# Optimization experiments

Hardware: AMD Instinct MI355X
Metric: run time of the kernel (lower is better)

Reference implementation:

```python
import jax, jax.numpy as jnp
import numpy as np

DELTA_V = 0.5
DELTA_D = 1.5
ALPHA = 1.0
BETA = 1.0
GAMMA = 0.001
K = 33  # label ids 0..32; 0 = background (ignored)
EPS = 1e-12


def setup_inputs() -> dict:
    key = jax.random.key(0)
    k1, k2 = jax.random.split(key)
    B, N, E = 8, 65536, 32
    embeddings = jax.random.normal(k1, (B, N, E), dtype=jnp.float32)
    labels = jax.random.randint(k2, (B, N), 0, K)
    return {"embeddings": embeddings, "labels": labels}


def reference(embeddings, labels):
    B, N, E = embeddings.shape
    dt = embeddings.dtype
    seg = (labels + jnp.arange(B)[:, None] * K).reshape(-1)  # (B*N,)

    # segment mean -> per-instance centers (B, K, E)
    sums = jax.ops.segment_sum(embeddings.reshape(B * N, E), seg, num_segments=B * K).reshape(B, K, E)
    counts = jax.ops.segment_sum(jnp.ones((B * N,), dtype=dt), seg, num_segments=B * K).reshape(B, K)
    centers = sums / jnp.maximum(counts, 1.0)[..., None]

    present = counts > 0
    present = present.at[:, 0].set(False)  # drop background label 0
    presf = present.astype(dt)
    n_inst = presf.sum(axis=1)  # (B,)

    # ---- variance term: per-point hinge distance to own center, segment-mean ----
    c_per_point = centers[jnp.arange(B)[:, None], labels]  # (B, N, E) gather
    d2 = ((embeddings - c_per_point) ** 2).sum(-1)
    dist = jnp.sqrt(jnp.maximum(d2, EPS))
    hinge = jnp.where(labels > 0, jnp.maximum(dist - DELTA_V, 0.0), 0.0)
    per_inst_sum = jax.ops.segment_sum(hinge.reshape(-1), seg, num_segments=B * K).reshape(B, K)
    per_inst_mean = per_inst_sum / jnp.maximum(counts, 1.0)
    variance_term = (per_inst_mean * presf).sum(1) / jnp.maximum(n_inst, 1.0)

    # ---- distance term: pairwise hinge between present instance centers ----
    diff2 = ((centers[:, :, None, :] - centers[:, None, :, :]) ** 2).sum(-1)  # (B,K,K)
    upper = jnp.triu(jnp.ones((K, K), dtype=bool), 1)[None]
    pair_valid = present[:, :, None] & present[:, None, :] & upper
    cd = jnp.sqrt(jnp.maximum(jnp.where(pair_valid, diff2, 1.0), EPS))
    pair_hinge = jnp.maximum(2.0 * DELTA_D - cd, 0.0) * pair_valid.astype(dt)
    n_pairs = n_inst * (n_inst - 1.0) * 0.5
    distance_term = pair_hinge.sum((1, 2)) / jnp.maximum(n_pairs, 1.0)

    # ---- regularization: mean L2 norm of present centers ----
    c_norm = jnp.sqrt(jnp.maximum((centers ** 2).sum(-1), EPS))
    reg_term = (c_norm * presf).sum(1) / jnp.maximum(n_inst, 1.0)

    per_batch = ALPHA * variance_term + BETA * distance_term + GAMMA * reg_term
    per_batch = jnp.where(n_inst > 0, per_batch, 0.0)
    return per_batch.sum() / B
```

## Files before the change

kernel.cpp:

```cpp
#include <hip/hip_runtime.h>
#include <math.h>

#define KC 33
#define ED 32
#define KE (KC * ED)
#define PAD 33

#define BPB_A 64
#define TPA 128
#define NSLOT 8
#define BPB_H 128
#define TPH 256


__global__ void k_zero(float* __restrict__ ws, int n, float* __restrict__ out) {
    int i = blockIdx.x * blockDim.x + threadIdx.x;
    if (i < n) ws[i] = 0.f;
    if (i == 0) out[0] = 0.f;
}

__global__ __launch_bounds__(256) void k_hist(const int* __restrict__ lab,
                                              float* __restrict__ counts, int N) {
    __shared__ float h[4 * KC];
    int t = threadIdx.x;
    int w = t >> 6;
    if (t < 4 * KC) h[t] = 0.f;
    __syncthreads();
    int b   = blockIdx.x >> 5;
    int blk = blockIdx.x & 31;
    const int4* l4 = (const int4*)(lab + (size_t)b * N + (size_t)blk * 2048);
    int4 a = l4[t];
    int4 c = l4[t + 256];
    float* hw = &h[w * KC];
    atomicAdd(&hw[a.x], 1.f); atomicAdd(&hw[a.y], 1.f);
    atomicAdd(&hw[a.z], 1.f); atomicAdd(&hw[a.w], 1.f);
    atomicAdd(&hw[c.x], 1.f); atomicAdd(&hw[c.y], 1.f);
    atomicAdd(&hw[c.z], 1.f); atomicAdd(&hw[c.w], 1.f);
    __syncthreads();
    if (t < KC)
        atomicAdd(&counts[b * KC + t], h[t] + h[KC + t] + h[2 * KC + t] + h[3 * KC + t]);
}

__global__ __launch_bounds__(256) void k_accum(const float* __restrict__ emb,
                                               const int* __restrict__ lab,
                                               float* __restrict__ sums, int N) {
    __shared__ float s_tile[TPA * PAD];
    __shared__ float s_priv[NSLOT * KE];
    __shared__ int   s_lab[TPA];
    int t = threadIdx.x;
    for (int i = t; i < NSLOT * KE; i += 256) s_priv[i] = 0.f;

    int b     = blockIdx.x / BPB_A;
    int blk   = blockIdx.x % BPB_A;
    int chunk = N / BPB_A;
    int e     = t & 31;
    int slot  = t >> 5;
    size_t pbase = (size_t)b * N + (size_t)blk * chunk;
    const int NT = chunk / TPA;

    const float4* g4 = (const float4*)(emb + pbase * ED);
    float4 r0 = g4[t], r1 = g4[t + 256], r2 = g4[t + 512], r3 = g4[t + 768];
    int rl = 0;
    if (t < TPA) rl = lab[pbase + t];
    __syncthreads();

    for (int tb = 0; tb < NT; tb++) {
        {
            int f, p, m;
            f = t;        p = f >> 3; m = (f & 7) * 4;
            { float* d = &s_tile[PAD * p + m]; d[0]=r0.x; d[1]=r0.y; d[2]=r0.z; d[3]=r0.w; }
            f = t + 256;  p = f >> 3; m = (f & 7) * 4;
            { float* d = &s_tile[PAD * p + m]; d[0]=r1.x; d[1]=r1.y; d[2]=r1.z; d[3]=r1.w; }
            f = t + 512;  p = f >> 3; m = (f & 7) * 4;
            { float* d = &s_tile[PAD * p + m]; d[0]=r2.x; d[1]=r2.y; d[2]=r2.z; d[3]=r2.w; }
            f = t + 768;  p = f >> 3; m = (f & 7) * 4;
            { float* d = &s_tile[PAD * p + m]; d[0]=r3.x; d[1]=r3.y; d[2]=r3.z; d[3]=r3.w; }
        }
        if (t < TPA) s_lab[t] = rl;
        __syncthreads();

        if (tb + 1 < NT) {
            const float4* gn = (const float4*)(emb + (pbase + (size_t)(tb + 1) * TPA) * ED);
            r0 = gn[t]; r1 = gn[t + 256]; r2 = gn[t + 512]; r3 = gn[t + 768];
            if (t < TPA) rl = lab[pbase + (size_t)(tb + 1) * TPA + t];
        }

        float* priv = &s_priv[slot * KE];
#pragma unroll
        for (int st = 0; st < TPA / NSLOT; st++) {
            int pt = st * NSLOT + slot;
            float x = s_tile[pt * PAD + e];
            int   k = s_lab[pt];
            priv[k * ED + e] += x;
        }
        __syncthreads();
    }

    for (int i = t; i < KE; i += 256) {
        float v = 0.f;
#pragma unroll
        for (int s = 0; s < NSLOT; s++) v += s_priv[s * KE + i];
        atomicAdd(&sums[(size_t)b * KE + i], v);
    }
}

__global__ __launch_bounds__(256) void k_hinge(const float* __restrict__ emb,
                                               const int* __restrict__ lab,
                                               const float* __restrict__ sums,
                                               const float* __restrict__ counts,
                                               float* __restrict__ var, int N) {
    __shared__ float s_tile[TPH * PAD];
    __shared__ float s_ctr[KC * PAD];
    __shared__ float s_cnt[KC];
    __shared__ float s_inv[KC];
    __shared__ int   s_lab[TPH];
    __shared__ float s_red[4];
    int t     = threadIdx.x;
    int b     = blockIdx.x / BPB_H;
    int blk   = blockIdx.x % BPB_H;
    int chunk = N / BPB_H;
    size_t pbase = (size_t)b * N + (size_t)blk * chunk;
    const int NT = chunk / TPH;

    const float4* g4 = (const float4*)(emb + pbase * ED);
    float4 r0 = g4[t],        r1 = g4[t + 256],  r2 = g4[t + 512],  r3 = g4[t + 768];
    float4 r4 = g4[t + 1024], r5 = g4[t + 1280], r6 = g4[t + 1536], r7 = g4[t + 1792];
    int rl = lab[pbase + t];

    if (t < KC) {
        float c = counts[b * KC + t];
        s_cnt[t] = fmaxf(c, 1.f);
        s_inv[t] = (t > 0 && c > 0.f) ? 1.f / fmaxf(c, 1.f) : 0.f;
    }
    __syncthreads();
    for (int i = t; i < KE; i += 256) {
        int k = i >> 5, e = i & 31;
        s_ctr[k * PAD + e] = sums[(size_t)b * KE + i] / s_cnt[k];
    }

    float hs = 0.f;
    for (int tb = 0; tb < NT; tb++) {
        {
            int f, p, m;
            f = t;         p = f >> 3; m = (f & 7) * 4;
            { float* d = &s_tile[PAD * p + m]; d[0]=r0.x; d[1]=r0.y; d[2]=r0.z; d[3]=r0.w; }
            f = t + 256;   p = f >> 3; m = (f & 7) * 4;
            { float* d = &s_tile[PAD * p + m]; d[0]=r1.x; d[1]=r1.y; d[2]=r1.z; d[3]=r1.w; }
            f = t + 512;   p = f >> 3; m = (f & 7) * 4;
            { float* d = &s_tile[PAD * p + m]; d[0]=r2.x; d[1]=r2.y; d[2]=r2.z; d[3]=r2.w; }
            f = t + 768;   p = f >> 3; m = (f & 7) * 4;
            { float* d = &s_tile[PAD * p + m]; d[0]=r3.x; d[1]=r3.y; d[2]=r3.z; d[3]=r3.w; }
            f = t + 1024;  p = f >> 3; m = (f & 7) * 4;
            { float* d = &s_tile[PAD * p + m]; d[0]=r4.x; d[1]=r4.y; d[2]=r4.z; d[3]=r4.w; }
            f = t + 1280;  p = f >> 3; m = (f & 7) * 4;
            { float* d = &s_tile[PAD * p + m]; d[0]=r5.x; d[1]=r5.y; d[2]=r5.z; d[3]=r5.w; }
            f = t + 1536;  p = f >> 3; m = (f & 7) * 4;
            { float* d = &s_tile[PAD * p + m]; d[0]=r6.x; d[1]=r6.y; d[2]=r6.z; d[3]=r6.w; }
            f = t + 1792;  p = f >> 3; m = (f & 7) * 4;
            { float* d = &s_tile[PAD * p + m]; d[0]=r7.x; d[1]=r7.y; d[2]=r7.z; d[3]=r7.w; }
        }
        s_lab[t] = rl;
        __syncthreads();

        if (tb + 1 < NT) {
            const float4* gn = (const float4*)(emb + (pbase + (size_t)(tb + 1) * TPH) * ED);
            r0 = gn[t];        r1 = gn[t + 256];  r2 = gn[t + 512];  r3 = gn[t + 768];
            r4 = gn[t + 1024]; r5 = gn[t + 1280]; r6 = gn[t + 1536]; r7 = gn[t + 1792];
            rl = lab[pbase + (size_t)(tb + 1) * TPH + t];
        }

        int   k  = s_lab[t];
        float iv = s_inv[k];
        const float* xr = &s_tile[t * PAD];
        const float* cr = &s_ctr[k * PAD];
        float d2 = 0.f;
#pragma unroll
        for (int j = 0; j < ED; j++) {
            float d = xr[j] - cr[j];
            d2 = fmaf(d, d, d2);
        }
        float dist = sqrtf(fmaxf(d2, 1e-12f));
        hs += fmaxf(dist - 0.5f, 0.f) * iv;
        __syncthreads();
    }

    hs += __shfl_xor(hs, 1);  hs += __shfl_xor(hs, 2);  hs += __shfl_xor(hs, 4);
    hs += __shfl_xor(hs, 8);  hs += __shfl_xor(hs, 16); hs += __shfl_xor(hs, 32);
    if ((t & 63) == 0) s_red[t >> 6] = hs;
    __syncthreads();
    if (t == 0)
        atomicAdd(&var[b], s_red[0] + s_red[1] + s_red[2] + s_red[3]);
}

__global__ __launch_bounds__(256) void k_final(const float* __restrict__ sums,
                                               const float* __restrict__ counts,
                                               const float* __restrict__ var,
                                               float* __restrict__ out, int B) {
    __shared__ float s_ctr[KE];
    __shared__ float s_cnt[KC];
    __shared__ float s_reg[KC];
    __shared__ int   s_prs[KC];
    __shared__ float s_red[256];
    int b = blockIdx.x;
    int t = threadIdx.x;

    if (t < KC) {
        float c = counts[b * KC + t];
        s_cnt[t] = fmaxf(c, 1.f);
        s_prs[t] = (t > 0 && c > 0.f) ? 1 : 0;
    }
    __syncthreads();
    for (int i = t; i < KE; i += 256)
        s_ctr[i] = sums[(size_t)b * KE + i] / s_cnt[i >> 5];
    __syncthreads();
    if (t < KC) {
        float n2 = 0.f;
        for (int e2 = 0; e2 < ED; e2++) { float c = s_ctr[t * ED + e2]; n2 += c * c; }
        s_reg[t] = s_prs[t] ? sqrtf(fmaxf(n2, 1e-12f)) : 0.f;
    }
    __syncthreads();

    float psum = 0.f;
    for (int q = t; q < KC * KC; q += 256) {
        int i = q / KC, j = q % KC;
        if (i < j && s_prs[i] && s_prs[j]) {
            float d2 = 0.f;
            for (int e2 = 0; e2 < ED; e2++) {
                float d = s_ctr[i * ED + e2] - s_ctr[j * ED + e2];
                d2 += d * d;
            }
            float cd = sqrtf(fmaxf(d2, 1e-12f));
            psum += fmaxf(3.0f - cd, 0.f);
        }
    }
    s_red[t] = psum;
    __syncthreads();
    for (int s = 128; s > 0; s >>= 1) {
        if (t < s) s_red[t] += s_red[t + s];
        __syncthreads();
    }

    if (t == 0) {
        float reg = 0.f; int n = 0;
        for (int k = 0; k < KC; k++) { reg += s_reg[k]; n += s_prs[k]; }
        float nf = (float)n;
        float variance_term = var[b] / fmaxf(nf, 1.f);
        float npairs = nf * (nf - 1.f) * 0.5f;
        float distance_term = s_red[0] / fmaxf(npairs, 1.f);
        float reg_term = reg / fmaxf(nf, 1.f);
        float pb = variance_term + distance_term + 0.001f * reg_term;
        if (n == 0) pb = 0.f;
        atomicAdd(out, pb / (float)B);
    }
}

extern "C" void kernel_launch(void* const* d_in, const int* in_sizes, int n_in,
                              void* d_out, int out_size, void* d_ws, size_t ws_size,
                              hipStream_t stream) {
    const float* emb = (const float*)d_in[0];
    const int*   lab = (const int*)d_in[1];
    float* out = (float*)d_out;

    const int B = 8;
    const int N = in_sizes[1] / B;

    float* sums   = (float*)d_ws;
    float* counts = sums + (size_t)B * KE;
    float* var    = counts + (size_t)B * KC;

    int zn = B * KE + B * KC + B;
    k_zero<<<(zn + 255) / 256, 256, 0, stream>>>(sums, zn, out);
    k_hist<<<B * 32, 256, 0, stream>>>(lab, counts, N);
    k_accum<<<B * BPB_A, 256, 0, stream>>>(emb, lab, sums, N);
    k_hinge<<<B * BPB_H, 256, 0, stream>>>(emb, lab, sums, counts, var, N);
    k_final<<<B, 256, 0, stream>>>(sums, counts, var, out, B);
}
```

Measured before the change: 133.4 us.

## Fuse histogram into accumulation, finalize via last-block, drop hinge LDS staging

The label histogram moves into the accumulation kernel, and the separate final kernel is replaced by a last-block-done counter inside the hinge kernel, which removes two launches. The hinge kernel now loads each point's 32 floats straight into registers (8 float4 per thread) and double-buffers them across iterations. This drops the shared-memory tile, its transposed stores and the per-iteration barriers. In exchange, per-thread strided loads are less coalesced, register pressure rises, and the fused finalize adds a threadfence and atomic counter.

```diff
diff --git a/kernel.cpp b/kernel.cpp
--- a/kernel.cpp
+++ b/kernel.cpp
@@ -19,36 +19,17 @@
     if (i == 0) out[0] = 0.f;
 }
 
-__global__ __launch_bounds__(256) void k_hist(const int* __restrict__ lab,
-                                              float* __restrict__ counts, int N) {
-    __shared__ float h[4 * KC];
-    int t = threadIdx.x;
-    int w = t >> 6;
-    if (t < 4 * KC) h[t] = 0.f;
-    __syncthreads();
-    int b   = blockIdx.x >> 5;
-    int blk = blockIdx.x & 31;
-    const int4* l4 = (const int4*)(lab + (size_t)b * N + (size_t)blk * 2048);
-    int4 a = l4[t];
-    int4 c = l4[t + 256];
-    float* hw = &h[w * KC];
-    atomicAdd(&hw[a.x], 1.f); atomicAdd(&hw[a.y], 1.f);
-    atomicAdd(&hw[a.z], 1.f); atomicAdd(&hw[a.w], 1.f);
-    atomicAdd(&hw[c.x], 1.f); atomicAdd(&hw[c.y], 1.f);
-    atomicAdd(&hw[c.z], 1.f); atomicAdd(&hw[c.w], 1.f);
-    __syncthreads();
-    if (t < KC)
-        atomicAdd(&counts[b * KC + t], h[t] + h[KC + t] + h[2 * KC + t] + h[3 * KC + t]);
-}
-
 __global__ __launch_bounds__(256) void k_accum(const float* __restrict__ emb,
                                                const int* __restrict__ lab,
-                                               float* __restrict__ sums, int N) {
+                                               float* __restrict__ sums,
+                                               float* __restrict__ counts, int N) {
     __shared__ float s_tile[TPA * PAD];
     __shared__ float s_priv[NSLOT * KE];
     __shared__ int   s_lab[TPA];
+    __shared__ float s_hist[2 * KC];
     int t = threadIdx.x;
     for (int i = t; i < NSLOT * KE; i += 256) s_priv[i] = 0.f;
+    if (t < 2 * KC) s_hist[t] = 0.f;
 
     int b     = blockIdx.x / BPB_A;
     int blk   = blockIdx.x % BPB_A;
@@ -76,7 +57,10 @@
             f = t + 768;  p = f >> 3; m = (f & 7) * 4;
             { float* d = &s_tile[PAD * p + m]; d[0]=r3.x; d[1]=r3.y; d[2]=r3.z; d[3]=r3.w; }
         }
-        if (t < TPA) s_lab[t] = rl;
+        if (t < TPA) {
+            s_lab[t] = rl;
+            atomicAdd(&s_hist[(t >> 6) * KC + rl], 1.f);
+        }
         __syncthreads();
 
         if (tb + 1 < NT) {
@@ -102,19 +86,32 @@
         for (int s = 0; s < NSLOT; s++) v += s_priv[s * KE + i];
         atomicAdd(&sums[(size_t)b * KE + i], v);
     }
-}
+    if (t < KC)
+        atomicAdd(&counts[b * KC + t], s_hist[t] + s_hist[KC + t]);
+}
+
+#define D2ACC(v, o) { float d_;                          \
+    d_ = (v).x - cr[(o)];     d2 = fmaf(d_, d_, d2);     \
+    d_ = (v).y - cr[(o) + 1]; d2 = fmaf(d_, d_, d2);     \
+    d_ = (v).z - cr[(o) + 2]; d2 = fmaf(d_, d_, d2);     \
+    d_ = (v).w - cr[(o) + 3]; d2 = fmaf(d_, d_, d2); }
 
 __global__ __launch_bounds__(256) void k_hinge(const float* __restrict__ emb,
                                                const int* __restrict__ lab,
                                                const float* __restrict__ sums,
                                                const float* __restrict__ counts,
-                                               float* __restrict__ var, int N) {
-    __shared__ float s_tile[TPH * PAD];
+                                               float* __restrict__ var,
+                                               unsigned* __restrict__ done,
+                                               float* __restrict__ out,
+                                               int N, int B) {
     __shared__ float s_ctr[KC * PAD];
     __shared__ float s_cnt[KC];
     __shared__ float s_inv[KC];
-    __shared__ int   s_lab[TPH];
+    __shared__ int   s_prs[KC];
+    __shared__ float s_reg[KC];
     __shared__ float s_red[4];
+    __shared__ float s_red2[256];
+    __shared__ int   s_last;
     int t     = threadIdx.x;
     int b     = blockIdx.x / BPB_H;
     int blk   = blockIdx.x % BPB_H;
@@ -122,100 +119,66 @@
     size_t pbase = (size_t)b * N + (size_t)blk * chunk;
     const int NT = chunk / TPH;
 
-    const float4* g4 = (const float4*)(emb + pbase * ED);
-    float4 r0 = g4[t],        r1 = g4[t + 256],  r2 = g4[t + 512],  r3 = g4[t + 768];
-    float4 r4 = g4[t + 1024], r5 = g4[t + 1280], r6 = g4[t + 1536], r7 = g4[t + 1792];
-    int rl = lab[pbase + t];
+    const float4* g0 = (const float4*)(emb + (pbase + t) * ED);
+    float4 x0 = g0[0], x1 = g0[1], x2 = g0[2], x3 = g0[3],
+           x4 = g0[4], x5 = g0[5], x6 = g0[6], x7 = g0[7];
+    int rk = lab[pbase + t];
 
     if (t < KC) {
         float c = counts[b * KC + t];
         s_cnt[t] = fmaxf(c, 1.f);
-        s_inv[t] = (t > 0 && c > 0.f) ? 1.f / fmaxf(c, 1.f) : 0.f;
+        int p = (t > 0 && c > 0.f) ? 1 : 0;
+        s_inv[t] = p ? 1.f / fmaxf(c, 1.f) : 0.f;
+        s_prs[t] = p;
     }
     __syncthreads();
     for (int i = t; i < KE; i += 256) {
         int k = i >> 5, e = i & 31;
         s_ctr[k * PAD + e] = sums[(size_t)b * KE + i] / s_cnt[k];
     }
+    __syncthreads();
 
     float hs = 0.f;
     for (int tb = 0; tb < NT; tb++) {
-        {
-            int f, p, m;
-            f = t;         p = f >> 3; m = (f & 7) * 4;
-            { float* d = &s_tile[PAD * p + m]; d[0]=r0.x; d[1]=r0.y; d[2]=r0.z; d[3]=r0.w; }
-            f = t + 256;   p = f >> 3; m = (f & 7) * 4;
-            { float* d = &s_tile[PAD * p + m]; d[0]=r1.x; d[1]=r1.y; d[2]=r1.z; d[3]=r1.w; }
-            f = t + 512;   p = f >> 3; m = (f & 7) * 4;
-            { float* d = &s_tile[PAD * p + m]; d[0]=r2.x; d[1]=r2.y; d[2]=r2.z; d[3]=r2.w; }
-            f = t + 768;   p = f >> 3; m = (f & 7) * 4;
-            { float* d = &s_tile[PAD * p + m]; d[0]=r3.x; d[1]=r3.y; d[2]=r3.z; d[3]=r3.w; }
-            f = t + 1024;  p = f >> 3; m = (f & 7) * 4;
-            { float* d = &s_tile[PAD * p + m]; d[0]=r4.x; d[1]=r4.y; d[2]=r4.z; d[3]=r4.w; }
-            f = t + 1280;  p = f >> 3; m = (f & 7) * 4;
-            { float* d = &s_tile[PAD * p + m]; d[0]=r5.x; d[1]=r5.y; d[2]=r5.z; d[3]=r5.w; }
-            f = t + 1536;  p = f >> 3; m = (f & 7) * 4;
-            { float* d = &s_tile[PAD * p + m]; d[0]=r6.x; d[1]=r6.y; d[2]=r6.z; d[3]=r6.w; }
-            f = t + 1792;  p = f >> 3; m = (f & 7) * 4;
-            { float* d = &s_tile[PAD * p + m]; d[0]=r7.x; d[1]=r7.y; d[2]=r7.z; d[3]=r7.w; }
-        }
-        s_lab[t] = rl;
-        __syncthreads();
-
+        float4 y0, y1, y2, y3, y4, y5, y6, y7;
+        int nk = 0;
         if (tb + 1 < NT) {
-            const float4* gn = (const float4*)(emb + (pbase + (size_t)(tb + 1) * TPH) * ED);
-            r0 = gn[t];        r1 = gn[t + 256];  r2 = gn[t + 512];  r3 = gn[t + 768];
-            r4 = gn[t + 1024]; r5 = gn[t + 1280]; r6 = gn[t + 1536]; r7 = gn[t + 1792];
-            rl = lab[pbase + (size_t)(tb + 1) * TPH + t];
-        }
-
-        int   k  = s_lab[t];
-        float iv = s_inv[k];
-        const float* xr = &s_tile[t * PAD];
-        const float* cr = &s_ctr[k * PAD];
+            const float4* gn = (const float4*)(emb + (pbase + (size_t)(tb + 1) * TPH + t) * ED);
+            y0 = gn[0]; y1 = gn[1]; y2 = gn[2]; y3 = gn[3];
+            y4 = gn[4]; y5 = gn[5]; y6 = gn[6]; y7 = gn[7];
+            nk = lab[pbase + (size_t)(tb + 1) * TPH + t];
+        }
+        const float* cr = &s_ctr[rk * PAD];
+        float iv = s_inv[rk];
         float d2 = 0.f;
-#pragma unroll
-        for (int j = 0; j < ED; j++) {
-            float d = xr[j] - cr[j];
-            d2 = fmaf(d, d, d2);
-        }
+        D2ACC(x0, 0)  D2ACC(x1, 4)  D2ACC(x2, 8)  D2ACC(x3, 12)
+        D2ACC(x4, 16) D2ACC(x5, 20) D2ACC(x6, 24) D2ACC(x7, 28)
         float dist = sqrtf(fmaxf(d2, 1e-12f));
         hs += fmaxf(dist - 0.5f, 0.f) * iv;
-        __syncthreads();
+        if (tb + 1 < NT) {
+            x0 = y0; x1 = y1; x2 = y2; x3 = y3;
+            x4 = y4; x5 = y5; x6 = y6; x7 = y7;
+            rk = nk;
+        }
     }
 
     hs += __shfl_xor(hs, 1);  hs += __shfl_xor(hs, 2);  hs += __shfl_xor(hs, 4);
     hs += __shfl_xor(hs, 8);  hs += __shfl_xor(hs, 16); hs += __shfl_xor(hs, 32);
     if ((t & 63) == 0) s_red[t >> 6] = hs;
     __syncthreads();
-    if (t == 0)
+    if (t == 0) {
         atomicAdd(&var[b], s_red[0] + s_red[1] + s_red[2] + s_red[3]);
-}
-
-__global__ __launch_bounds__(256) void k_final(const float* __restrict__ sums,
-                                               const float* __restrict__ counts,
-                                               const float* __restrict__ var,
-                                               float* __restrict__ out, int B) {
-    __shared__ float s_ctr[KE];
-    __shared__ float s_cnt[KC];
-    __shared__ float s_reg[KC];
-    __shared__ int   s_prs[KC];
-    __shared__ float s_red[256];
-    int b = blockIdx.x;
-    int t = threadIdx.x;
-
-    if (t < KC) {
-        float c = counts[b * KC + t];
-        s_cnt[t] = fmaxf(c, 1.f);
-        s_prs[t] = (t > 0 && c > 0.f) ? 1 : 0;
-    }
-    __syncthreads();
-    for (int i = t; i < KE; i += 256)
-        s_ctr[i] = sums[(size_t)b * KE + i] / s_cnt[i >> 5];
-    __syncthreads();
+        __threadfence();
+        unsigned old = atomicAdd(&done[b], 1u);
+        s_last = (old == (unsigned)(BPB_H - 1)) ? 1 : 0;
+    }
+    __syncthreads();
+    if (!s_last) return;
+
+    __threadfence();
     if (t < KC) {
         float n2 = 0.f;
-        for (int e2 = 0; e2 < ED; e2++) { float c = s_ctr[t * ED + e2]; n2 += c * c; }
+        for (int e2 = 0; e2 < ED; e2++) { float c = s_ctr[t * PAD + e2]; n2 += c * c; }
         s_reg[t] = s_prs[t] ? sqrtf(fmaxf(n2, 1e-12f)) : 0.f;
     }
     __syncthreads();
@@ -226,27 +189,28 @@
         if (i < j && s_prs[i] && s_prs[j]) {
             float d2 = 0.f;
             for (int e2 = 0; e2 < ED; e2++) {
-                float d = s_ctr[i * ED + e2] - s_ctr[j * ED + e2];
+                float d = s_ctr[i * PAD + e2] - s_ctr[j * PAD + e2];
                 d2 += d * d;
             }
             float cd = sqrtf(fmaxf(d2, 1e-12f));
             psum += fmaxf(3.0f - cd, 0.f);
         }
     }
-    s_red[t] = psum;
+    s_red2[t] = psum;
     __syncthreads();
     for (int s = 128; s > 0; s >>= 1) {
-        if (t < s) s_red[t] += s_red[t + s];
+        if (t < s) s_red2[t] += s_red2[t + s];
         __syncthreads();
     }
 
     if (t == 0) {
+        float vb = atomicAdd(&var[b], 0.f);
         float reg = 0.f; int n = 0;
         for (int k = 0; k < KC; k++) { reg += s_reg[k]; n += s_prs[k]; }
         float nf = (float)n;
-        float variance_term = var[b] / fmaxf(nf, 1.f);
+        float variance_term = vb / fmaxf(nf, 1.f);
         float npairs = nf * (nf - 1.f) * 0.5f;
-        float distance_term = s_red[0] / fmaxf(npairs, 1.f);
+        float distance_term = s_red2[0] / fmaxf(npairs, 1.f);
         float reg_term = reg / fmaxf(nf, 1.f);
         float pb = variance_term + distance_term + 0.001f * reg_term;
         if (n == 0) pb = 0.f;
@@ -264,14 +228,13 @@
     const int B = 8;
     const int N = in_sizes[1] / B;
 
-    float* sums   = (float*)d_ws;
-    float* counts = sums + (size_t)B * KE;
-    float* var    = counts + (size_t)B * KC;
-
-    int zn = B * KE + B * KC + B;
-    k_zero<<<(zn + 255) / 256, 256, 0, stream>>>(sums, zn, out);
-    k_hist<<<B * 32, 256, 0, stream>>>(lab, counts, N);
-    k_accum<<<B * BPB_A, 256, 0, stream>>>(emb, lab, sums, N);
-    k_hinge<<<B * BPB_H, 256, 0, stream>>>(emb, lab, sums, counts, var, N);
-    k_final<<<B, 256, 0, stream>>>(sums, counts, var, out, B);
-}
+    float*    sums   = (float*)d_ws;
+    float*    counts = sums + (size_t)B * KE;
+    float*    var    = counts + (size_t)B * KC;
+    unsigned* done   = (unsigned*)(var + B);
+
+    int zn = B * KE + B * KC + B + B;
+    k_zero<<<(zn + 255) / 256, 256, 0, stream>>>((float*)d_ws, zn, out);
+    k_accum<<<B * BPB_A, 256, 0, stream>>>(emb, lab, sums, counts, N);
+    k_hinge<<<B * BPB_H, 256, 0, stream>>>(emb, lab, sums, counts, var, done, out, N, B);
+}
```

After: 155.7 us. +16.7%, slower.
